# Optimization experiments

Measured on AMD Instinct MI355X. Metric: run time of the kernel, lower is better.

The kernel has to match this reference:

```python
import jax, jax.numpy as jnp
import numpy as np

N, H, B = 500000, 256, 1024

def setup_inputs() -> dict:
    key = jax.random.key(0)
    k1, k2, k3, k4 = jax.random.split(key, 4)
    x = jax.random.normal(k1, (N, H), dtype=jnp.float32)
    W = jax.random.normal(k2, (H, H), dtype=jnp.float32) * (1.0 / np.sqrt(H))
    b = jax.random.normal(k3, (H,), dtype=jnp.float32) * 0.02
    seg_ids = jnp.sort(jax.random.randint(k4, (N,), 0, B))
    return {"x": x, "seg_ids": seg_ids, "W": W, "b": b, "num_segments": B}

def reference(x, seg_ids, W, b, num_segments):
    # per-node linear: [N,H] @ [H,H]^T + b  (matches nn.Linear)
    h = x @ W.T + b
    # sum-pool per graph (segment sum), then ReLU -> [B, H]
    pooled = jax.ops.segment_sum(h, seg_ids, num_segments=num_segments)
    return jax.nn.relu(pooled)
```

## Files before the change

### kernel.cpp

```cpp
#include <hip/hip_runtime.h>

#define HDIM 256
#define ROWS_PER_WAVE 128
#define GEMM_ROWS 16

__global__ __launch_bounds__(256) void seg_pool_kernel(
    const float* __restrict__ x, const int* __restrict__ seg,
    float* __restrict__ pooled, float* __restrict__ counts, int N)
{
    const int wave = blockIdx.x * (blockDim.x >> 6) + (threadIdx.x >> 6);
    const int lane = threadIdx.x & 63;

    long r0 = (long)wave * ROWS_PER_WAVE;
    if (r0 >= N) return;
    long r1 = r0 + ROWS_PER_WAVE;
    if (r1 > N) r1 = N;

    float4 acc = make_float4(0.f, 0.f, 0.f, 0.f);
    int cur = seg[r0];
    int cnt = 0;

    long r = r0;
    while (r < r1) {
        if (r + 4 <= r1) {
            int sA = seg[r];
            int sB = seg[r + 3];
            if (sA == cur && sB == cur) {
                const float4* p = (const float4*)(x + r * HDIM) + lane;
                float4 v0 = p[0];
                float4 v1 = p[64];
                float4 v2 = p[128];
                float4 v3 = p[192];
                acc.x += (v0.x + v1.x) + (v2.x + v3.x);
                acc.y += (v0.y + v1.y) + (v2.y + v3.y);
                acc.z += (v0.z + v1.z) + (v2.z + v3.z);
                acc.w += (v0.w + v1.w) + (v2.w + v3.w);
                cnt += 4;
                r += 4;
                continue;
            }
        }
        int s = seg[r];
        if (s != cur) {
            float* dst = pooled + (long)cur * HDIM + lane * 4;
            atomicAdd(dst + 0, acc.x);
            atomicAdd(dst + 1, acc.y);
            atomicAdd(dst + 2, acc.z);
            atomicAdd(dst + 3, acc.w);
            if (lane == 0) atomicAdd(&counts[cur], (float)cnt);
            acc = make_float4(0.f, 0.f, 0.f, 0.f);
            cnt = 0;
            cur = s;
        }
        const float4* p = (const float4*)(x + r * HDIM) + lane;
        float4 v = *p;
        acc.x += v.x; acc.y += v.y; acc.z += v.z; acc.w += v.w;
        ++cnt;
        ++r;
    }
    if (cnt > 0) {
        float* dst = pooled + (long)cur * HDIM + lane * 4;
        atomicAdd(dst + 0, acc.x);
        atomicAdd(dst + 1, acc.y);
        atomicAdd(dst + 2, acc.z);
        atomicAdd(dst + 3, acc.w);
        if (lane == 0) atomicAdd(&counts[cur], (float)cnt);
    }
}

__global__ __launch_bounds__(256) void transpose_kernel(
    const float* __restrict__ W, float* __restrict__ Wt)
{
    __shared__ float tile[32][33];
    const int tx = threadIdx.x & 31;
    const int ty = threadIdx.x >> 5;
    const int bx = blockIdx.x;
    const int by = blockIdx.y;
#pragma unroll
    for (int i = 0; i < 32; i += 8)
        tile[ty + i][tx] = W[(by * 32 + ty + i) * HDIM + bx * 32 + tx];
    __syncthreads();
#pragma unroll
    for (int i = 0; i < 32; i += 8)
        Wt[(bx * 32 + ty + i) * HDIM + by * 32 + tx] = tile[tx][ty + i];
}

__global__ __launch_bounds__(256) void out_gemm_kernel(
    const float* __restrict__ pooled, const float* __restrict__ Wt,
    const float* __restrict__ bias, const float* __restrict__ counts,
    float* __restrict__ out, int B)
{
    __shared__ float sp[GEMM_ROWS][HDIM];
    const int col = threadIdx.x;
    const int r0 = blockIdx.x * GEMM_ROWS;
    const int rmax = (B - r0 < GEMM_ROWS) ? (B - r0) : GEMM_ROWS;

    for (int r = 0; r < rmax; ++r)
        sp[r][col] = pooled[(long)(r0 + r) * HDIM + col];
    __syncthreads();

    float acc[GEMM_ROWS];
#pragma unroll
    for (int r = 0; r < GEMM_ROWS; ++r) acc[r] = 0.f;

    for (int k = 0; k < HDIM; ++k) {
        float w = Wt[(long)k * HDIM + col];
#pragma unroll
        for (int r = 0; r < GEMM_ROWS; ++r)
            acc[r] = fmaf(sp[r][k], w, acc[r]);
    }

    float bv = bias[col];
    for (int r = 0; r < rmax; ++r) {
        float v = acc[r] + counts[r0 + r] * bv;
        out[(long)(r0 + r) * HDIM + col] = fmaxf(v, 0.f);
    }
}

extern "C" void kernel_launch(void* const* d_in, const int* in_sizes, int n_in,
                              void* d_out, int out_size, void* d_ws, size_t ws_size,
                              hipStream_t stream)
{
    const float* x   = (const float*)d_in[0];
    const int*   seg = (const int*)d_in[1];
    const float* W   = (const float*)d_in[2];
    const float* b   = (const float*)d_in[3];
    float*       out = (float*)d_out;

    const int N = in_sizes[0] / HDIM;
    const int B = out_size / HDIM;

    float* pooled = (float*)d_ws;
    float* counts = pooled + (size_t)B * HDIM;
    float* Wt     = counts + B;

    hipMemsetAsync(d_ws, 0, ((size_t)B * HDIM + B) * sizeof(float), stream);

    const int waves  = (N + ROWS_PER_WAVE - 1) / ROWS_PER_WAVE;
    const int blocks = (waves + 3) / 4;
    seg_pool_kernel<<<blocks, 256, 0, stream>>>(x, seg, pooled, counts, N);

    transpose_kernel<<<dim3(HDIM / 32, HDIM / 32), 256, 0, stream>>>(W, Wt);

    const int gblocks = (B + GEMM_ROWS - 1) / GEMM_ROWS;
    out_gemm_kernel<<<gblocks, 256, 0, stream>>>(pooled, Wt, b, counts, out, B);
}
```

Baseline: 704.7 us.

## Preload segment ids via shuffles, fast-path uniform chunks, fuse memset into transpose

The pooling kernel now loads each wave's 128 segment ids once with coalesced lane loads and reads them with shuffles. A chunk whose first and last ids match takes an unrolled 8-row accumulation path with no per-row id checks. The workspace memset is folded into the transpose kernel, which removes a launch. The output GEMM drops to 4 rows per block for more blocks and uses vectorized shared-memory reads. The main cost is still streaming the 512MB input, so the gains are limited to issue overhead and launch count. The zero-fill relies on B*HDIM+B being divisible by 4.

```diff
diff --git a/kernel.cpp b/kernel.cpp
--- a/kernel.cpp
+++ b/kernel.cpp
@@ -2,74 +2,105 @@
 
 #define HDIM 256
 #define ROWS_PER_WAVE 128
-#define GEMM_ROWS 16
+#define GEMM_ROWS 4
+
+__device__ __forceinline__ void flush_acc(float* __restrict__ pooled,
+                                          float* __restrict__ counts,
+                                          int segid, int lane,
+                                          const float4& acc, int cnt)
+{
+    float* dst = pooled + (long)segid * HDIM + lane * 4;
+    atomicAdd(dst + 0, acc.x);
+    atomicAdd(dst + 1, acc.y);
+    atomicAdd(dst + 2, acc.z);
+    atomicAdd(dst + 3, acc.w);
+    if (lane == 0) atomicAdd(&counts[segid], (float)cnt);
+}
 
 __global__ __launch_bounds__(256) void seg_pool_kernel(
     const float* __restrict__ x, const int* __restrict__ seg,
     float* __restrict__ pooled, float* __restrict__ counts, int N)
 {
-    const int wave = blockIdx.x * (blockDim.x >> 6) + (threadIdx.x >> 6);
+    const int wave = blockIdx.x * 4 + (threadIdx.x >> 6);
     const int lane = threadIdx.x & 63;
 
     long r0 = (long)wave * ROWS_PER_WAVE;
     if (r0 >= N) return;
     long r1 = r0 + ROWS_PER_WAVE;
     if (r1 > N) r1 = N;
+    const int nrows = (int)(r1 - r0);
+
+    long i0 = r0 + lane;       if (i0 >= N) i0 = N - 1;
+    long i1 = r0 + 64 + lane;  if (i1 >= N) i1 = N - 1;
+    const int sv0 = seg[i0];
+    const int sv1 = seg[i1];
+    const int sfirst = __shfl(sv0, 0);
+    const int slast  = (nrows <= 64) ? __shfl(sv0, nrows - 1)
+                                     : __shfl(sv1, nrows - 1 - 64);
+
+    const float4* xp = (const float4*)x + r0 * 64 + lane;
 
     float4 acc = make_float4(0.f, 0.f, 0.f, 0.f);
-    int cur = seg[r0];
-    int cnt = 0;
 
-    long r = r0;
-    while (r < r1) {
-        if (r + 4 <= r1) {
-            int sA = seg[r];
-            int sB = seg[r + 3];
-            if (sA == cur && sB == cur) {
-                const float4* p = (const float4*)(x + r * HDIM) + lane;
-                float4 v0 = p[0];
-                float4 v1 = p[64];
-                float4 v2 = p[128];
-                float4 v3 = p[192];
-                acc.x += (v0.x + v1.x) + (v2.x + v3.x);
-                acc.y += (v0.y + v1.y) + (v2.y + v3.y);
-                acc.z += (v0.z + v1.z) + (v2.z + v3.z);
-                acc.w += (v0.w + v1.w) + (v2.w + v3.w);
-                cnt += 4;
-                r += 4;
-                continue;
+    if (sfirst == slast) {
+        int rr = 0;
+        for (; rr + 8 <= nrows; rr += 8) {
+            float4 v0 = xp[(rr + 0) * 64];
+            float4 v1 = xp[(rr + 1) * 64];
+            float4 v2 = xp[(rr + 2) * 64];
+            float4 v3 = xp[(rr + 3) * 64];
+            float4 v4 = xp[(rr + 4) * 64];
+            float4 v5 = xp[(rr + 5) * 64];
+            float4 v6 = xp[(rr + 6) * 64];
+            float4 v7 = xp[(rr + 7) * 64];
+            acc.x += ((v0.x + v1.x) + (v2.x + v3.x)) + ((v4.x + v5.x) + (v6.x + v7.x));
+            acc.y += ((v0.y + v1.y) + (v2.y + v3.y)) + ((v4.y + v5.y) + (v6.y + v7.y));
+            acc.z += ((v0.z + v1.z) + (v2.z + v3.z)) + ((v4.z + v5.z) + (v6.z + v7.z));
+            acc.w += ((v0.w + v1.w) + (v2.w + v3.w)) + ((v4.w + v5.w) + (v6.w + v7.w));
+        }
+        for (; rr < nrows; ++rr) {
+            float4 v = xp[rr * 64];
+            acc.x += v.x; acc.y += v.y; acc.z += v.z; acc.w += v.w;
+        }
+        flush_acc(pooled, counts, sfirst, lane, acc, nrows);
+    } else {
+        int cur = sfirst;
+        int cnt = 0;
+        int rr  = 0;
+        while (rr < nrows) {
+            int s_r = (rr < 64) ? __shfl(sv0, rr) : __shfl(sv1, rr - 64);
+            if (s_r != cur) {
+                flush_acc(pooled, counts, cur, lane, acc, cnt);
+                acc = make_float4(0.f, 0.f, 0.f, 0.f);
+                cnt = 0;
+                cur = s_r;
             }
+            if (rr + 4 <= nrows) {
+                int s_3 = (rr + 3 < 64) ? __shfl(sv0, rr + 3) : __shfl(sv1, rr + 3 - 64);
+                if (s_3 == cur) {
+                    float4 v0 = xp[(rr + 0) * 64];
+                    float4 v1 = xp[(rr + 1) * 64];
+                    float4 v2 = xp[(rr + 2) * 64];
+                    float4 v3 = xp[(rr + 3) * 64];
+                    acc.x += (v0.x + v1.x) + (v2.x + v3.x);
+                    acc.y += (v0.y + v1.y) + (v2.y + v3.y);
+                    acc.z += (v0.z + v1.z) + (v2.z + v3.z);
+                    acc.w += (v0.w + v1.w) + (v2.w + v3.w);
+                    cnt += 4; rr += 4;
+                    continue;
+                }
+            }
+            float4 v = xp[rr * 64];
+            acc.x += v.x; acc.y += v.y; acc.z += v.z; acc.w += v.w;
+            ++cnt; ++rr;
         }
-        int s = seg[r];
-        if (s != cur) {
-            float* dst = pooled + (long)cur * HDIM + lane * 4;
-            atomicAdd(dst + 0, acc.x);
-            atomicAdd(dst + 1, acc.y);
-            atomicAdd(dst + 2, acc.z);
-            atomicAdd(dst + 3, acc.w);
-            if (lane == 0) atomicAdd(&counts[cur], (float)cnt);
-            acc = make_float4(0.f, 0.f, 0.f, 0.f);
-            cnt = 0;
-            cur = s;
-        }
-        const float4* p = (const float4*)(x + r * HDIM) + lane;
-        float4 v = *p;
-        acc.x += v.x; acc.y += v.y; acc.z += v.z; acc.w += v.w;
-        ++cnt;
-        ++r;
-    }
-    if (cnt > 0) {
-        float* dst = pooled + (long)cur * HDIM + lane * 4;
-        atomicAdd(dst + 0, acc.x);
-        atomicAdd(dst + 1, acc.y);
-        atomicAdd(dst + 2, acc.z);
-        atomicAdd(dst + 3, acc.w);
-        if (lane == 0) atomicAdd(&counts[cur], (float)cnt);
+        flush_acc(pooled, counts, cur, lane, acc, cnt);
     }
 }
 
-__global__ __launch_bounds__(256) void transpose_kernel(
-    const float* __restrict__ W, float* __restrict__ Wt)
+__global__ __launch_bounds__(256) void prep_kernel(
+    const float* __restrict__ W, float* __restrict__ Wt,
+    float4* __restrict__ zero_dst, int zero_count4)
 {
     __shared__ float tile[32][33];
     const int tx = threadIdx.x & 31;
@@ -79,6 +110,12 @@
 #pragma unroll
     for (int i = 0; i < 32; i += 8)
         tile[ty + i][tx] = W[(by * 32 + ty + i) * HDIM + bx * 32 + tx];
+
+    const int gtid = (blockIdx.y * gridDim.x + blockIdx.x) * 256 + threadIdx.x;
+    const int nth  = gridDim.x * gridDim.y * 256;
+    const float4 z = make_float4(0.f, 0.f, 0.f, 0.f);
+    for (int i = gtid; i < zero_count4; i += nth) zero_dst[i] = z;
+
     __syncthreads();
 #pragma unroll
     for (int i = 0; i < 32; i += 8)
@@ -92,27 +129,37 @@
 {
     __shared__ float sp[GEMM_ROWS][HDIM];
     const int col = threadIdx.x;
-    const int r0 = blockIdx.x * GEMM_ROWS;
+    const int r0  = blockIdx.x * GEMM_ROWS;
     const int rmax = (B - r0 < GEMM_ROWS) ? (B - r0) : GEMM_ROWS;
 
-    for (int r = 0; r < rmax; ++r)
-        sp[r][col] = pooled[(long)(r0 + r) * HDIM + col];
+    {
+        const float4* src = (const float4*)(pooled + (long)r0 * HDIM);
+        float4* dst = (float4*)&sp[0][0];
+        int lim = rmax * (HDIM / 4);
+        dst[col] = (col < lim) ? src[col] : make_float4(0.f, 0.f, 0.f, 0.f);
+    }
     __syncthreads();
 
-    float acc[GEMM_ROWS];
-#pragma unroll
-    for (int r = 0; r < GEMM_ROWS; ++r) acc[r] = 0.f;
-
-    for (int k = 0; k < HDIM; ++k) {
-        float w = Wt[(long)k * HDIM + col];
-#pragma unroll
-        for (int r = 0; r < GEMM_ROWS; ++r)
-            acc[r] = fmaf(sp[r][k], w, acc[r]);
+    float a0 = 0.f, a1 = 0.f, a2 = 0.f, a3 = 0.f;
+    for (int k = 0; k < HDIM; k += 4) {
+        float w0 = Wt[(long)(k + 0) * HDIM + col];
+        float w1 = Wt[(long)(k + 1) * HDIM + col];
+        float w2 = Wt[(long)(k + 2) * HDIM + col];
+        float w3 = Wt[(long)(k + 3) * HDIM + col];
+        float4 s0 = *(const float4*)&sp[0][k];
+        float4 s1 = *(const float4*)&sp[1][k];
+        float4 s2 = *(const float4*)&sp[2][k];
+        float4 s3 = *(const float4*)&sp[3][k];
+        a0 = fmaf(s0.x, w0, a0); a0 = fmaf(s0.y, w1, a0); a0 = fmaf(s0.z, w2, a0); a0 = fmaf(s0.w, w3, a0);
+        a1 = fmaf(s1.x, w0, a1); a1 = fmaf(s1.y, w1, a1); a1 = fmaf(s1.z, w2, a1); a1 = fmaf(s1.w, w3, a1);
+        a2 = fmaf(s2.x, w0, a2); a2 = fmaf(s2.y, w1, a2); a2 = fmaf(s2.z, w2, a2); a2 = fmaf(s2.w, w3, a2);
+        a3 = fmaf(s3.x, w0, a3); a3 = fmaf(s3.y, w1, a3); a3 = fmaf(s3.z, w2, a3); a3 = fmaf(s3.w, w3, a3);
     }
 
-    float bv = bias[col];
+    const float bv = bias[col];
+    float accs[GEMM_ROWS] = {a0, a1, a2, a3};
     for (int r = 0; r < rmax; ++r) {
-        float v = acc[r] + counts[r0 + r] * bv;
+        float v = accs[r] + counts[r0 + r] * bv;
         out[(long)(r0 + r) * HDIM + col] = fmaxf(v, 0.f);
     }
 }
@@ -134,14 +181,14 @@
     float* counts = pooled + (size_t)B * HDIM;
     float* Wt     = counts + B;
 
-    hipMemsetAsync(d_ws, 0, ((size_t)B * HDIM + B) * sizeof(float), stream);
+    const int zero_count4 = (B * HDIM + B) / 4;
+    prep_kernel<<<dim3(HDIM / 32, HDIM / 32), 256, 0, stream>>>(
+        W, Wt, (float4*)d_ws, zero_count4);
 
     const int waves  = (N + ROWS_PER_WAVE - 1) / ROWS_PER_WAVE;
     const int blocks = (waves + 3) / 4;
     seg_pool_kernel<<<blocks, 256, 0, stream>>>(x, seg, pooled, counts, N);
 
-    transpose_kernel<<<dim3(HDIM / 32, HDIM / 32), 256, 0, stream>>>(W, Wt);
-
     const int gblocks = (B + GEMM_ROWS - 1) / GEMM_ROWS;
     out_gemm_kernel<<<gblocks, 256, 0, stream>>>(pooled, Wt, b, counts, out, B);
 }
```

Measured after the change: 681.8 us. 3.3% less time.
